# Kernel optimization log

Measured on AMD Instinct MI355X. Metric: run time of the kernel, lower is better.

## Reference

```python
import jax, jax.numpy as jnp
import numpy as np

B, N, D, H, NC = 4, 32, 128, 8, 27
DK = D // H
DFF = 4 * D
L = NC * N


def layer_norm(x, g, b, eps=1e-5):
    mu = jnp.mean(x, -1, keepdims=True)
    var = jnp.var(x, -1, keepdims=True)
    return (x - mu) * jax.lax.rsqrt(var + eps) * g + b


def setup_inputs() -> dict:
    ks = jax.random.split(jax.random.key(0), 16)
    s = 1.0 / np.sqrt(D)
    return {
        'x': jax.random.normal(ks[0], (B, N, D), jnp.float32),
        'mask': jax.random.randint(ks[1], (B, 1, N), 0, 2, jnp.int32),
        'coords': jax.random.normal(ks[2], (B, NC, N, 3), jnp.float32),
        'Wp': jax.random.normal(ks[3], (3, D), jnp.float32) * 0.5,
        'bp': jnp.zeros((D,), jnp.float32),
        'Wq': jax.random.normal(ks[4], (D, D), jnp.float32) * s,
        'bq': jnp.zeros((D,), jnp.float32),
        'Wk': jax.random.normal(ks[5], (D, D), jnp.float32) * s,
        'bk': jnp.zeros((D,), jnp.float32),
        'Wv': jax.random.normal(ks[6], (D, D), jnp.float32) * s,
        'bv': jnp.zeros((D,), jnp.float32),
        'Wo': jax.random.normal(ks[7], (D, D), jnp.float32) * s,
        'bo': jnp.zeros((D,), jnp.float32),
        'g1': jnp.ones((D,), jnp.float32),
        'b1': jnp.zeros((D,), jnp.float32),
        'g2': jnp.ones((D,), jnp.float32),
        'b2': jnp.zeros((D,), jnp.float32),
        'W1': jax.random.normal(ks[8], (D, DFF), jnp.float32) * s,
        'bf1': jnp.zeros((DFF,), jnp.float32),
        'W2': jax.random.normal(ks[9], (DFF, D), jnp.float32) * (1.0 / np.sqrt(DFF)),
        'bf2': jnp.zeros((D,), jnp.float32),
    }


def reference(x, mask, coords, Wp, bp, Wq, bq, Wk, bk, Wv, bv, Wo, bo,
              g1, b1, g2, b2, W1, bf1, W2, bf2):
    mask_enh = jnp.tile(mask, (1, NC, 1)).reshape(B, 1, 1, L)

    def step(i):
        # position_encoding: x broadcast over 27 images + linear of coords relative to atom i
        ci = jax.lax.dynamic_slice_in_dim(coords, i, 1, axis=2)        # [B,NC,1,3]
        ar = x[:, None] + (coords - ci) @ Wp + bp                      # [B,NC,N,D]
        a = ar.reshape(B, L, D)
        hn = layer_norm(a, g1, b1)
        q = (hn @ Wq + bq).reshape(B, L, H, DK).transpose(0, 2, 1, 3)
        k = (hn @ Wk + bk).reshape(B, L, H, DK).transpose(0, 2, 1, 3)
        v = (hn @ Wv + bv).reshape(B, L, H, DK).transpose(0, 2, 1, 3)
        scores = jnp.einsum('bhqd,bhkd->bhqk', q, k) / np.sqrt(DK)     # [B,H,L,L]
        scores = jnp.where(mask_enh == 0, -1e9, scores)
        att = jnp.einsum('bhqk,bhkd->bhqd', jax.nn.softmax(scores, -1), v)
        att = att.transpose(0, 2, 1, 3).reshape(B, L, D) @ Wo + bo
        s = a + att  # SublayerConnection (dropout identity in eval)
        # original keeps only [b, image 0, atom i] of the [B,NC,N,D] reshape; flat index = i
        return jax.lax.dynamic_slice_in_dim(s, i, 1, axis=1)[:, 0]     # [B,D]

    rows = jax.lax.map(step, jnp.arange(N))                            # [N,B,D]
    y = rows.transpose(1, 0, 2)                                        # [B,N,D]
    hn2 = layer_norm(y, g2, b2)
    return y + (jax.nn.relu(hn2 @ W1 + bf1) @ W2 + bf2)
```

## Files before the change

kernel.cpp:

```cpp
#include <hip/hip_runtime.h>


#define B_ 4
#define N_ 32
#define D_ 128
#define H_ 8
#define NC_ 27
#define DFF_ 512
#define L_ (NC_*N_)

__device__ __forceinline__ float wave_red_sum(float v){
  #pragma unroll
  for (int off = 32; off; off >>= 1) v += __shfl_xor(v, off);
  return v;
}

__device__ __forceinline__ void bred2(float& a, float& b, float sred[2][8][2],
                                      int tid, int phase){
  for (int off = 32; off; off >>= 1){ a += __shfl_xor(a, off); b += __shfl_xor(b, off); }
  int pb = phase & 1;
  if ((tid & 63) == 0){ sred[pb][tid>>6][0] = a; sred[pb][tid>>6][1] = b; }
  __syncthreads();
  float sa = 0.f, sb = 0.f;
  #pragma unroll
  for (int w = 0; w < 8; w++){ sa += sred[pb][w][0]; sb += sred[pb][w][1]; }
  a = sa; b = sb;
}

__global__ __launch_bounds__(512) void k_fused(
    const float* __restrict__ x, const int* __restrict__ mask,
    const float* __restrict__ coords,
    const float* __restrict__ Wp, const float* __restrict__ bp,
    const float* __restrict__ Wq, const float* __restrict__ bq,
    const float* __restrict__ Wk, const float* __restrict__ bk,
    const float* __restrict__ Wv, const float* __restrict__ bv,
    const float* __restrict__ Wo, const float* __restrict__ bo,
    const float* __restrict__ g1, const float* __restrict__ b1,
    const float* __restrict__ g2, const float* __restrict__ b2,
    const float* __restrict__ W1, const float* __restrict__ bf1,
    const float* __restrict__ W2, const float* __restrict__ bfb2,
    float* __restrict__ out)
{
  __shared__ float sc_s[H_*L_];
  __shared__ float is_s[L_];
  __shared__ float dc_s[3][L_];
  __shared__ float xh_s[N_][D_+1];
  __shared__ float ZU_s[H_][D_+4];
  __shared__ float w_s[3][D_];
  __shared__ float g1_s[D_], b1_s[D_], bp_s[D_];
  __shared__ float q_s[D_];
  __shared__ float hn_s[D_];
  __shared__ float qAxk_s[H_][N_];
  __shared__ float qGk_s[H_][3];
  __shared__ float S3_s[H_];
  __shared__ float varx_s[N_];
  __shared__ float dxp_s[N_][3];
  __shared__ int   mask_s[N_];
  __shared__ float cq_s[NC_][3];
  __shared__ float M6_s[6];
  __shared__ float mwp_s[3];
  __shared__ float Tnp_s[H_][2][N_];
  __shared__ float Sh_s[H_], RD_s[H_][3];
  __shared__ float att_s[D_], y_s[D_], f_s[DFF_];
  __shared__ float po[4][D_];
  __shared__ float sred[2][8][2];

  int bi = blockIdx.x;
  int b = bi >> 5, i = bi & 31;
  int tid  = threadIdx.x;
  int wave = tid >> 6, lane = tid & 63;

  if (tid < 384) w_s[tid>>7][tid&127] = Wp[tid];
  if (tid < D_){ g1_s[tid] = g1[tid]; b1_s[tid] = b1[tid]; bp_s[tid] = bp[tid]; }
  if (tid >= 384 && tid < 384+N_) mask_s[tid-384] = mask[b*N_ + (tid-384)];
  if (tid >= 416 && tid < 416+NC_*3){
    int t2 = tid - 416;
    cq_s[t2/3][t2%3] = coords[((size_t)(b*NC_ + t2/3)*N_ + i)*3 + t2%3];
  }
  __syncthreads();
  if (wave < 3){
    float s = w_s[wave][lane] + w_s[wave][lane+64];
    s = wave_red_sum(s);
    if (lane == 0) mwp_s[wave] = s*(1.f/D_);
  }
  __syncthreads();
  if (tid < 384) w_s[tid>>7][tid&127] -= mwp_s[tid>>7];
  __syncthreads();
  if (wave < 6){
    const int ja[6] = {0,0,0,1,1,2}, jb[6] = {0,1,2,1,2,2};
    float s = w_s[ja[wave]][lane]*w_s[jb[wave]][lane]
            + w_s[ja[wave]][lane+64]*w_s[jb[wave]][lane+64];
    s = wave_red_sum(s);
    if (lane == 0) M6_s[wave] = s;
  }

  for (int r = wave; r < N_; r += 8){
    float t0 = x[((size_t)(b*N_+r))*D_ + lane]     + bp_s[lane];
    float t1 = x[((size_t)(b*N_+r))*D_ + lane+64]  + bp_s[lane+64];
    float mean = wave_red_sum(t0 + t1)*(1.f/D_);
    float xh0 = t0 - mean, xh1 = t1 - mean;
    xh_s[r][lane] = xh0; xh_s[r][lane+64] = xh1;
    float vv = xh0*xh0 + xh1*xh1;
    float d0 = xh0*w_s[0][lane] + xh1*w_s[0][lane+64];
    float d1 = xh0*w_s[1][lane] + xh1*w_s[1][lane+64];
    float d2 = xh0*w_s[2][lane] + xh1*w_s[2][lane+64];
    #pragma unroll
    for (int off = 32; off; off >>= 1){
      vv += __shfl_xor(vv, off); d0 += __shfl_xor(d0, off);
      d1 += __shfl_xor(d1, off); d2 += __shfl_xor(d2, off);
    }
    if (lane == 0){
      varx_s[r] = vv*(1.f/D_);
      dxp_s[r][0] = d0; dxp_s[r][1] = d1; dxp_s[r][2] = d2;
    }
  }
  __syncthreads();

  if (tid < D_){
    float isq = rsqrtf(varx_s[i] + 1e-5f);
    hn_s[tid] = xh_s[i][tid]*isq*g1_s[tid] + b1_s[tid];
  }
  __syncthreads();
  {
    int slot = tid >> 7, d = tid & 127;
    float a = 0.f;
    #pragma unroll 8
    for (int e = slot*32; e < slot*32+32; e++) a += hn_s[e]*Wq[e*D_+d];
    po[slot][d] = a;
  }
  __syncthreads();
  if (tid < D_) q_s[tid] = po[0][tid]+po[1][tid]+po[2][tid]+po[3][tid] + bq[tid];
  __syncthreads();

  {
    int e = tid & 127, h0 = tid >> 7;
    #pragma unroll
    for (int hh = 0; hh < 2; hh++){
      int h = h0 + hh*4;
      const float4* wk4 = (const float4*)(Wk + (size_t)e*D_ + h*16);
      float s = 0.f;
      #pragma unroll
      for (int kq = 0; kq < 4; kq++){
        float4 wv4 = wk4[kq];
        s += wv4.x*q_s[h*16+kq*4+0] + wv4.y*q_s[h*16+kq*4+1]
           + wv4.z*q_s[h*16+kq*4+2] + wv4.w*q_s[h*16+kq*4+3];
      }
      ZU_s[h][e] = s;
    }
  }
  __syncthreads();
  {
    int h = wave;
    float u0 = ZU_s[h][lane], u1 = ZU_s[h][lane+64];
    float s3 = b1_s[lane]*u0 + b1_s[lane+64]*u1;
    if (lane < 16) s3 += q_s[h*16+lane]*bk[h*16+lane];
    float qg0 = w_s[0][lane]*g1_s[lane]*u0 + w_s[0][lane+64]*g1_s[lane+64]*u1;
    float qg1 = w_s[1][lane]*g1_s[lane]*u0 + w_s[1][lane+64]*g1_s[lane+64]*u1;
    float qg2 = w_s[2][lane]*g1_s[lane]*u0 + w_s[2][lane+64]*g1_s[lane+64]*u1;
    #pragma unroll
    for (int off = 32; off; off >>= 1){
      s3  += __shfl_xor(s3,  off); qg0 += __shfl_xor(qg0, off);
      qg1 += __shfl_xor(qg1, off); qg2 += __shfl_xor(qg2, off);
    }
    if (lane == 0){ S3_s[h]=s3; qGk_s[h][0]=qg0; qGk_s[h][1]=qg1; qGk_s[h][2]=qg2; }
  }
  __syncthreads();
  {
    int e = tid & 127, h0 = tid >> 7;
    ZU_s[h0][e]   *= g1_s[e];
    ZU_s[h0+4][e] *= g1_s[e];
  }
  __syncthreads();
  {
    int half = tid >> 8, id = tid & 255, h = id >> 5, n = id & 31;
    float s = 0.f;
    #pragma unroll 8
    for (int e = half*64; e < half*64+64; e++) s += xh_s[n][e]*ZU_s[h][e];
    ((float*)po)[half*256 + id] = s;
  }
  __syncthreads();
  if (tid < 256){
    int h = tid >> 5, n = tid & 31;
    qAxk_s[h][n] = ((float*)po)[tid] + ((float*)po)[256 + tid];
  }
  __syncthreads();

  for (int l = tid; l < L_; l += 512){
    int c = l >> 5, n = l & 31;
    const float* ck = coords + ((size_t)(b*NC_+c)*N_ + n)*3;
    float d0 = ck[0]-cq_s[c][0], d1 = ck[1]-cq_s[c][1], d2 = ck[2]-cq_s[c][2];
    dc_s[0][l] = d0; dc_s[1][l] = d1; dc_s[2][l] = d2;
    float quad = d0*d0*M6_s[0] + d1*d1*M6_s[3] + d2*d2*M6_s[5]
               + 2.f*(d0*d1*M6_s[1] + d0*d2*M6_s[2] + d1*d2*M6_s[4]);
    float lin  = d0*dxp_s[n][0] + d1*dxp_s[n][1] + d2*dxp_s[n][2];
    float E = varx_s[n] + (quad + 2.f*lin)*(1.f/D_);
    float is = rsqrtf(fmaxf(E, 0.f) + 1e-5f);
    is_s[l] = is;
    bool mk = mask_s[n] != 0;
    #pragma unroll
    for (int h = 0; h < H_; h++){
      float sc = 0.25f*(is*(qAxk_s[h][n]
                 + d0*qGk_s[h][0] + d1*qGk_s[h][1] + d2*qGk_s[h][2]) + S3_s[h]);
      sc_s[h*L_ + l] = mk ? sc : -1e9f;
    }
  }
  __syncthreads();

  {
    int h = tid >> 6, n = lane & 31, half = lane >> 5;
    int c0 = half ? 14 : 0, c1 = half ? NC_ : 14;
    float M = -3.0e38f;
    for (int c = c0; c < c1; c++) M = fmaxf(M, sc_s[h*L_ + c*N_ + n]);
    #pragma unroll
    for (int off = 32; off; off >>= 1) M = fmaxf(M, __shfl_xor(M, off));
    float S=0.f, Tn=0.f, r0=0.f, r1=0.f, r2=0.f;
    for (int c = c0; c < c1; c++){
      int l = c*N_ + n;
      float w = expf(sc_s[h*L_ + l] - M);
      float t = w * is_s[l];
      S += w; Tn += t;
      r0 += t*dc_s[0][l]; r1 += t*dc_s[1][l]; r2 += t*dc_s[2][l];
    }
    Tnp_s[h][half][n] = Tn;
    #pragma unroll
    for (int off = 32; off; off >>= 1){
      S  += __shfl_xor(S,  off);
      r0 += __shfl_xor(r0, off);
      r1 += __shfl_xor(r1, off);
      r2 += __shfl_xor(r2, off);
    }
    if (lane == 0){ Sh_s[h]=S; RD_s[h][0]=r0; RD_s[h][1]=r1; RD_s[h][2]=r2; }
  }
  __syncthreads();

  {
    int e = tid & 127, h0 = tid >> 7;
    #pragma unroll
    for (int hh = 0; hh < 2; hh++){
      int h = h0 + hh*4;
      float z = 0.f;
      #pragma unroll 8
      for (int n = 0; n < N_; n++){
        float Tn = Tnp_s[h][0][n] + Tnp_s[h][1][n];
        z += Tn * xh_s[n][e];
      }
      z += RD_s[h][0]*w_s[0][e] + RD_s[h][1]*w_s[1][e] + RD_s[h][2]*w_s[2][e];
      float rS = 1.f / fmaxf(Sh_s[h], 1e-30f);
      ZU_s[h][e] = z*g1_s[e]*rS + b1_s[e];
    }
  }
  __syncthreads();

  {
    int slot = tid >> 7, d = tid & 127, h = d >> 4;
    float a = 0.f;
    #pragma unroll 8
    for (int e = slot*32; e < slot*32+32; e++) a += ZU_s[h][e]*Wv[e*D_+d];
    po[slot][d] = a;
  }
  __syncthreads();
  if (tid < D_) att_s[tid] = po[0][tid]+po[1][tid]+po[2][tid]+po[3][tid] + bv[tid];
  __syncthreads();

  {
    int slot = tid >> 7, d = tid & 127;
    float a = 0.f;
    #pragma unroll 8
    for (int e = slot*32; e < slot*32+32; e++) a += att_s[e]*Wo[e*D_+d];
    po[slot][d] = a;
  }
  __syncthreads();
  float yv = 0.f;
  if (tid < D_){
    yv = x[(size_t)bi*D_+tid] + bp_s[tid] + bo[tid]
       + po[0][tid]+po[1][tid]+po[2][tid]+po[3][tid];
    y_s[tid] = yv;
  }
  float s1 = (tid < D_) ? yv : 0.f, dm = 0.f;
  bred2(s1, dm, sred, tid, 0);
  float dev = yv - s1*(1.f/D_);
  float v1 = (tid < D_) ? dev*dev : 0.f; dm = 0.f;
  bred2(v1, dm, sred, tid, 1);
  if (tid < D_) hn_s[tid] = dev*rsqrtf(v1*(1.f/D_)+1e-5f)*g2[tid] + b2[tid];
  __syncthreads();
  float f = bf1[tid];
  #pragma unroll 8
  for (int e = 0; e < D_; e++) f += hn_s[e]*W1[e*DFF_+tid];
  f_s[tid] = fmaxf(f, 0.f);
  __syncthreads();
  {
    int slot = tid >> 7, d = tid & 127;
    float a = 0.f;
    #pragma unroll 8
    for (int j = slot*128; j < slot*128+128; j++) a += f_s[j]*W2[j*D_+d];
    po[slot][d] = a;
  }
  __syncthreads();
  if (tid < D_)
    out[(size_t)bi*D_+tid] = y_s[tid] + bfb2[tid]
                   + po[0][tid]+po[1][tid]+po[2][tid]+po[3][tid];
}

extern "C" void kernel_launch(void* const* d_in, const int* in_sizes, int n_in,
                              void* d_out, int out_size, void* d_ws, size_t ws_size,
                              hipStream_t stream){
  const float* x      = (const float*)d_in[0];
  const int*   mask   = (const int*)  d_in[1];
  const float* coords = (const float*)d_in[2];
  const float* Wp     = (const float*)d_in[3];
  const float* bp     = (const float*)d_in[4];
  const float* Wq     = (const float*)d_in[5];
  const float* bq     = (const float*)d_in[6];
  const float* Wk     = (const float*)d_in[7];
  const float* bk     = (const float*)d_in[8];
  const float* Wv     = (const float*)d_in[9];
  const float* bv     = (const float*)d_in[10];
  const float* Wo     = (const float*)d_in[11];
  const float* bo     = (const float*)d_in[12];
  const float* g1     = (const float*)d_in[13];
  const float* b1     = (const float*)d_in[14];
  const float* g2     = (const float*)d_in[15];
  const float* b2     = (const float*)d_in[16];
  const float* W1     = (const float*)d_in[17];
  const float* bf1    = (const float*)d_in[18];
  const float* W2     = (const float*)d_in[19];
  const float* bfb2   = (const float*)d_in[20];

  k_fused<<<B_*N_, 512, 0, stream>>>(x, mask, coords, Wp, bp, Wq, bq, Wk, bk,
                                     Wv, bv, Wo, bo, g1, b1, g2, b2,
                                     W1, bf1, W2, bfb2, (float*)d_out);
}
```

Measured before the change: 125.6 us.

## Double block size to 1024 threads and merge dependent phases to cut barriers

Raises the fused kernel from 512 to 1024 threads per block and redistributes every phase (matvec K-splits into 8 slots, softmax split into 4 chunks per head with a separate max pass) across the extra waves. All global loads for x, coords and the small parameter vectors are issued up front into registers or shared memory. Several sequential barriered steps are merged: g1 is folded into xg/wcg, and the Wp mean is removed algebraically via P6. LayerNorm2 moves to a single wave. This is meant to shorten the serial latency chain of a 128-block kernel that underfills the GPU, at the cost of more registers per block and an extra barrier for the two-pass softmax max.

Measured after the change: 117.6 us. 1.07x faster.

```diff
diff --git a/kernel.cpp b/kernel.cpp
--- a/kernel.cpp
+++ b/kernel.cpp
@@ -9,25 +9,13 @@
 #define DFF_ 512
 #define L_ (NC_*N_)
 
-__device__ __forceinline__ float wave_red_sum(float v){
+__device__ __forceinline__ float wred(float v){
   #pragma unroll
   for (int off = 32; off; off >>= 1) v += __shfl_xor(v, off);
   return v;
 }
 
-__device__ __forceinline__ void bred2(float& a, float& b, float sred[2][8][2],
-                                      int tid, int phase){
-  for (int off = 32; off; off >>= 1){ a += __shfl_xor(a, off); b += __shfl_xor(b, off); }
-  int pb = phase & 1;
-  if ((tid & 63) == 0){ sred[pb][tid>>6][0] = a; sred[pb][tid>>6][1] = b; }
-  __syncthreads();
-  float sa = 0.f, sb = 0.f;
-  #pragma unroll
-  for (int w = 0; w < 8; w++){ sa += sred[pb][w][0]; sb += sred[pb][w][1]; }
-  a = sa; b = sb;
-}
-
-__global__ __launch_bounds__(512) void k_fused(
+__global__ __launch_bounds__(1024) void k_fused(
     const float* __restrict__ x, const int* __restrict__ mask,
     const float* __restrict__ coords,
     const float* __restrict__ Wp, const float* __restrict__ bp,
@@ -44,12 +32,13 @@
   __shared__ float sc_s[H_*L_];
   __shared__ float is_s[L_];
   __shared__ float dc_s[3][L_];
-  __shared__ float xh_s[N_][D_+1];
-  __shared__ float ZU_s[H_][D_+4];
+  __shared__ float xg_s[N_][D_+1];
+  __shared__ float zz_s[H_][D_+1];
   __shared__ float w_s[3][D_];
-  __shared__ float g1_s[D_], b1_s[D_], bp_s[D_];
-  __shared__ float q_s[D_];
-  __shared__ float hn_s[D_];
+  __shared__ float wcg_s[3][D_];
+  __shared__ float g1_s[D_], b1_s[D_], bp_s[D_], bq_s[D_], bk_s[D_];
+  __shared__ float g2_s[D_], b2_s[D_], bv_s[D_], bo_s[D_], bfb2_s[D_];
+  __shared__ float q_s[D_], hn_s[D_], hn2_s[D_], att_s[D_], y_s[D_];
   __shared__ float qAxk_s[H_][N_];
   __shared__ float qGk_s[H_][3];
   __shared__ float S3_s[H_];
@@ -57,248 +46,316 @@
   __shared__ float dxp_s[N_][3];
   __shared__ int   mask_s[N_];
   __shared__ float cq_s[NC_][3];
-  __shared__ float M6_s[6];
-  __shared__ float mwp_s[3];
+  __shared__ float M6_s[6], mwp_s[3], P6_s[6];
+  __shared__ float pmax_s[H_][2];
   __shared__ float Tnp_s[H_][2][N_];
-  __shared__ float Sh_s[H_], RD_s[H_][3];
-  __shared__ float att_s[D_], y_s[D_], f_s[DFF_];
-  __shared__ float po[4][D_];
-  __shared__ float sred[2][8][2];
+  __shared__ float Sp_s[H_][2], RDp_s[H_][2][3];
+  __shared__ float f_s[DFF_];
+  __shared__ float po[8][D_];
 
   int bi = blockIdx.x;
   int b = bi >> 5, i = bi & 31;
-  int tid  = threadIdx.x;
-  int wave = tid >> 6, lane = tid & 63;
-
+  int tid = threadIdx.x, wave = tid >> 6, lane = tid & 63;
+
+  int r0 = wave*2, r1 = wave*2+1;
+  float xa0 = x[(size_t)(b*N_+r0)*D_ + lane];
+  float xa1 = x[(size_t)(b*N_+r0)*D_ + lane+64];
+  float xb0 = x[(size_t)(b*N_+r1)*D_ + lane];
+  float xb1 = x[(size_t)(b*N_+r1)*D_ + lane+64];
+  float xi0 = 0.f, xi1 = 0.f;
+  if (wave == 0){ xi0 = x[(size_t)bi*D_+lane]; xi1 = x[(size_t)bi*D_+lane+64]; }
+  float ck0=0.f, ck1=0.f, ck2=0.f;
+  if (tid < L_){
+    int c = tid >> 5, n = tid & 31;
+    const float* ck = coords + ((size_t)(b*NC_+c)*N_ + n)*3;
+    ck0 = ck[0]; ck1 = ck[1]; ck2 = ck[2];
+  }
   if (tid < 384) w_s[tid>>7][tid&127] = Wp[tid];
-  if (tid < D_){ g1_s[tid] = g1[tid]; b1_s[tid] = b1[tid]; bp_s[tid] = bp[tid]; }
-  if (tid >= 384 && tid < 384+N_) mask_s[tid-384] = mask[b*N_ + (tid-384)];
-  if (tid >= 416 && tid < 416+NC_*3){
-    int t2 = tid - 416;
-    cq_s[t2/3][t2%3] = coords[((size_t)(b*NC_ + t2/3)*N_ + i)*3 + t2%3];
-  }
-  __syncthreads();
-  if (wave < 3){
-    float s = w_s[wave][lane] + w_s[wave][lane+64];
-    s = wave_red_sum(s);
-    if (lane == 0) mwp_s[wave] = s*(1.f/D_);
-  }
-  __syncthreads();
-  if (tid < 384) w_s[tid>>7][tid&127] -= mwp_s[tid>>7];
-  __syncthreads();
-  if (wave < 6){
-    const int ja[6] = {0,0,0,1,1,2}, jb[6] = {0,1,2,1,2,2};
-    float s = w_s[ja[wave]][lane]*w_s[jb[wave]][lane]
-            + w_s[ja[wave]][lane+64]*w_s[jb[wave]][lane+64];
-    s = wave_red_sum(s);
-    if (lane == 0) M6_s[wave] = s;
-  }
-
-  for (int r = wave; r < N_; r += 8){
-    float t0 = x[((size_t)(b*N_+r))*D_ + lane]     + bp_s[lane];
-    float t1 = x[((size_t)(b*N_+r))*D_ + lane+64]  + bp_s[lane+64];
-    float mean = wave_red_sum(t0 + t1)*(1.f/D_);
-    float xh0 = t0 - mean, xh1 = t1 - mean;
-    xh_s[r][lane] = xh0; xh_s[r][lane+64] = xh1;
-    float vv = xh0*xh0 + xh1*xh1;
-    float d0 = xh0*w_s[0][lane] + xh1*w_s[0][lane+64];
-    float d1 = xh0*w_s[1][lane] + xh1*w_s[1][lane+64];
-    float d2 = xh0*w_s[2][lane] + xh1*w_s[2][lane+64];
-    #pragma unroll
-    for (int off = 32; off; off >>= 1){
-      vv += __shfl_xor(vv, off); d0 += __shfl_xor(d0, off);
-      d1 += __shfl_xor(d1, off); d2 += __shfl_xor(d2, off);
-    }
-    if (lane == 0){
-      varx_s[r] = vv*(1.f/D_);
-      dxp_s[r][0] = d0; dxp_s[r][1] = d1; dxp_s[r][2] = d2;
-    }
+  if (tid < 128)                g2_s[tid]       = g2[tid];
+  else if (tid < 256)           b2_s[tid-128]   = b2[tid-128];
+  else if (tid < 384)           bv_s[tid-256]   = bv[tid-256];
+  else if (tid < 512){ int t=tid-384; g1_s[t]=g1[t]; bo_s[t]=bo[t]; }
+  else if (tid < 640){ int t=tid-512; b1_s[t]=b1[t]; bfb2_s[t]=bfb2[t]; }
+  else if (tid < 768){ int t=tid-640; bp_s[t]=bp[t]; bq_s[t]=bq[t]; }
+  else if (tid < 800)           mask_s[tid-768] = mask[b*N_ + (tid-768)];
+  else if (tid < 881){
+    int t = tid-800;
+    cq_s[t/3][t%3] = coords[((size_t)(b*NC_ + t/3)*N_ + i)*3 + t%3];
+  }
+  else if (tid < 1009)          bk_s[tid-881]   = bk[tid-881];
+  __syncthreads();
+
+  {
+    float t0 = xa0 + bp_s[lane], t1 = xa1 + bp_s[lane+64];
+    float mean = wred(t0+t1)*(1.f/D_);
+    float h0 = t0-mean, h1 = t1-mean;
+    xg_s[r0][lane]    = h0*g1_s[lane];
+    xg_s[r0][lane+64] = h1*g1_s[lane+64];
+    float vv = h0*h0 + h1*h1;
+    float d0 = h0*w_s[0][lane] + h1*w_s[0][lane+64];
+    float d1 = h0*w_s[1][lane] + h1*w_s[1][lane+64];
+    float d2 = h0*w_s[2][lane] + h1*w_s[2][lane+64];
+    #pragma unroll
+    for (int off=32; off; off>>=1){
+      vv += __shfl_xor(vv,off); d0 += __shfl_xor(d0,off);
+      d1 += __shfl_xor(d1,off); d2 += __shfl_xor(d2,off);
+    }
+    if (lane==0){ varx_s[r0]=vv*(1.f/D_);
+      dxp_s[r0][0]=d0; dxp_s[r0][1]=d1; dxp_s[r0][2]=d2; }
+    t0 = xb0 + bp_s[lane]; t1 = xb1 + bp_s[lane+64];
+    mean = wred(t0+t1)*(1.f/D_);
+    h0 = t0-mean; h1 = t1-mean;
+    xg_s[r1][lane]    = h0*g1_s[lane];
+    xg_s[r1][lane+64] = h1*g1_s[lane+64];
+    vv = h0*h0 + h1*h1;
+    d0 = h0*w_s[0][lane] + h1*w_s[0][lane+64];
+    d1 = h0*w_s[1][lane] + h1*w_s[1][lane+64];
+    d2 = h0*w_s[2][lane] + h1*w_s[2][lane+64];
+    #pragma unroll
+    for (int off=32; off; off>>=1){
+      vv += __shfl_xor(vv,off); d0 += __shfl_xor(d0,off);
+      d1 += __shfl_xor(d1,off); d2 += __shfl_xor(d2,off);
+    }
+    if (lane==0){ varx_s[r1]=vv*(1.f/D_);
+      dxp_s[r1][0]=d0; dxp_s[r1][1]=d1; dxp_s[r1][2]=d2; }
+  }
+  float dc0=0.f, dc1=0.f, dc2=0.f;
+  if (tid < L_){
+    int c = tid >> 5;
+    dc0 = ck0 - cq_s[c][0]; dc1 = ck1 - cq_s[c][1]; dc2 = ck2 - cq_s[c][2];
+    dc_s[0][tid]=dc0; dc_s[1][tid]=dc1; dc_s[2][tid]=dc2;
+  }
+  if (wave >= 8 && wave < 11){
+    int j = wave - 8;
+    float s = w_s[j][lane] + w_s[j][lane+64];
+    s = wred(s);
+    if (lane==0) mwp_s[j] = s*(1.f/D_);
+  }
+  if (wave >= 10){
+    int idx = wave - 10;
+    int ja = (idx>=3) + (idx>=5);
+    int jb = idx - (idx>=3)*2 - (idx>=5);
+    float s = w_s[ja][lane]*w_s[jb][lane] + w_s[ja][lane+64]*w_s[jb][lane+64];
+    s = wred(s);
+    if (lane==0) P6_s[idx] = s;
+  }
+  __syncthreads();
+
+  if (tid < 384){ int j=tid>>7, e=tid&127;
+    wcg_s[j][e] = (w_s[j][e] - mwp_s[j])*g1_s[e]; }
+  if (tid == 384){
+    M6_s[0]=P6_s[0]-D_*mwp_s[0]*mwp_s[0];
+    M6_s[1]=P6_s[1]-D_*mwp_s[0]*mwp_s[1];
+    M6_s[2]=P6_s[2]-D_*mwp_s[0]*mwp_s[2];
+    M6_s[3]=P6_s[3]-D_*mwp_s[1]*mwp_s[1];
+    M6_s[4]=P6_s[4]-D_*mwp_s[1]*mwp_s[2];
+    M6_s[5]=P6_s[5]-D_*mwp_s[2]*mwp_s[2];
+  }
+  if (tid >= 512 && tid < 640){ int e = tid-512;
+    hn_s[e] = xg_s[i][e]*rsqrtf(varx_s[i]+1e-5f) + b1_s[e]; }
+  __syncthreads();
+
+  {
+    int slot = tid>>7, d = tid&127;
+    float a = 0.f;
+    #pragma unroll
+    for (int e = slot*16; e < slot*16+16; e++) a += hn_s[e]*Wq[e*D_+d];
+    po[slot][d] = a;
   }
   __syncthreads();
 
   if (tid < D_){
-    float isq = rsqrtf(varx_s[i] + 1e-5f);
-    hn_s[tid] = xh_s[i][tid]*isq*g1_s[tid] + b1_s[tid];
-  }
-  __syncthreads();
-  {
-    int slot = tid >> 7, d = tid & 127;
-    float a = 0.f;
-    #pragma unroll 8
-    for (int e = slot*32; e < slot*32+32; e++) a += hn_s[e]*Wq[e*D_+d];
-    po[slot][d] = a;
-  }
-  __syncthreads();
-  if (tid < D_) q_s[tid] = po[0][tid]+po[1][tid]+po[2][tid]+po[3][tid] + bq[tid];
-  __syncthreads();
-
-  {
-    int e = tid & 127, h0 = tid >> 7;
-    #pragma unroll
-    for (int hh = 0; hh < 2; hh++){
-      int h = h0 + hh*4;
-      const float4* wk4 = (const float4*)(Wk + (size_t)e*D_ + h*16);
-      float s = 0.f;
-      #pragma unroll
-      for (int kq = 0; kq < 4; kq++){
-        float4 wv4 = wk4[kq];
-        s += wv4.x*q_s[h*16+kq*4+0] + wv4.y*q_s[h*16+kq*4+1]
-           + wv4.z*q_s[h*16+kq*4+2] + wv4.w*q_s[h*16+kq*4+3];
-      }
-      ZU_s[h][e] = s;
-    }
-  }
-  __syncthreads();
-  {
-    int h = wave;
-    float u0 = ZU_s[h][lane], u1 = ZU_s[h][lane+64];
-    float s3 = b1_s[lane]*u0 + b1_s[lane+64]*u1;
-    if (lane < 16) s3 += q_s[h*16+lane]*bk[h*16+lane];
-    float qg0 = w_s[0][lane]*g1_s[lane]*u0 + w_s[0][lane+64]*g1_s[lane+64]*u1;
-    float qg1 = w_s[1][lane]*g1_s[lane]*u0 + w_s[1][lane+64]*g1_s[lane+64]*u1;
-    float qg2 = w_s[2][lane]*g1_s[lane]*u0 + w_s[2][lane+64]*g1_s[lane+64]*u1;
-    #pragma unroll
-    for (int off = 32; off; off >>= 1){
-      s3  += __shfl_xor(s3,  off); qg0 += __shfl_xor(qg0, off);
-      qg1 += __shfl_xor(qg1, off); qg2 += __shfl_xor(qg2, off);
-    }
-    if (lane == 0){ S3_s[h]=s3; qGk_s[h][0]=qg0; qGk_s[h][1]=qg1; qGk_s[h][2]=qg2; }
-  }
-  __syncthreads();
-  {
-    int e = tid & 127, h0 = tid >> 7;
-    ZU_s[h0][e]   *= g1_s[e];
-    ZU_s[h0+4][e] *= g1_s[e];
-  }
-  __syncthreads();
-  {
-    int half = tid >> 8, id = tid & 255, h = id >> 5, n = id & 31;
+    float a = bq_s[tid];
+    #pragma unroll
+    for (int s=0;s<8;s++) a += po[s][tid];
+    q_s[tid] = a;
+  }
+  __syncthreads();
+
+  {
+    int h = tid>>7, e = tid&127;
+    const float4* wk4 = (const float4*)(Wk + (size_t)e*D_ + h*16);
+    float s = 0.f;
+    #pragma unroll
+    for (int kq=0; kq<4; kq++){
+      float4 w4 = wk4[kq];
+      s += w4.x*q_s[h*16+kq*4+0] + w4.y*q_s[h*16+kq*4+1]
+         + w4.z*q_s[h*16+kq*4+2] + w4.w*q_s[h*16+kq*4+3];
+    }
+    zz_s[h][e] = s;
+  }
+  __syncthreads();
+
+  {
+    int quarter = tid>>8, id = tid&255, h = id>>5, n = id&31;
     float s = 0.f;
     #pragma unroll 8
-    for (int e = half*64; e < half*64+64; e++) s += xh_s[n][e]*ZU_s[h][e];
-    ((float*)po)[half*256 + id] = s;
-  }
-  __syncthreads();
+    for (int e = quarter*32; e < quarter*32+32; e++) s += xg_s[n][e]*zz_s[h][e];
+    ((float*)po)[quarter*256 + id] = s;
+  }
+  __syncthreads();
+
   if (tid < 256){
-    int h = tid >> 5, n = tid & 31;
-    qAxk_s[h][n] = ((float*)po)[tid] + ((float*)po)[256 + tid];
-  }
-  __syncthreads();
-
-  for (int l = tid; l < L_; l += 512){
-    int c = l >> 5, n = l & 31;
-    const float* ck = coords + ((size_t)(b*NC_+c)*N_ + n)*3;
-    float d0 = ck[0]-cq_s[c][0], d1 = ck[1]-cq_s[c][1], d2 = ck[2]-cq_s[c][2];
-    dc_s[0][l] = d0; dc_s[1][l] = d1; dc_s[2][l] = d2;
-    float quad = d0*d0*M6_s[0] + d1*d1*M6_s[3] + d2*d2*M6_s[5]
-               + 2.f*(d0*d1*M6_s[1] + d0*d2*M6_s[2] + d1*d2*M6_s[4]);
-    float lin  = d0*dxp_s[n][0] + d1*dxp_s[n][1] + d2*dxp_s[n][2];
+    int h = tid>>5, n = tid&31;
+    qAxk_s[h][n] = ((float*)po)[tid] + ((float*)po)[256+tid]
+                 + ((float*)po)[512+tid] + ((float*)po)[768+tid];
+  }
+  if (wave >= 8){
+    int h = wave - 8;
+    float u0 = zz_s[h][lane], u1 = zz_s[h][lane+64];
+    float s3 = b1_s[lane]*u0 + b1_s[lane+64]*u1;
+    if (lane < 16) s3 += q_s[h*16+lane]*bk_s[h*16+lane];
+    float qg0 = wcg_s[0][lane]*u0 + wcg_s[0][lane+64]*u1;
+    float qg1 = wcg_s[1][lane]*u0 + wcg_s[1][lane+64]*u1;
+    float qg2 = wcg_s[2][lane]*u0 + wcg_s[2][lane+64]*u1;
+    #pragma unroll
+    for (int off=32; off; off>>=1){
+      s3  += __shfl_xor(s3,off);  qg0 += __shfl_xor(qg0,off);
+      qg1 += __shfl_xor(qg1,off); qg2 += __shfl_xor(qg2,off);
+    }
+    if (lane==0){ S3_s[h]=s3; qGk_s[h][0]=qg0; qGk_s[h][1]=qg1; qGk_s[h][2]=qg2; }
+  }
+  __syncthreads();
+
+  if (tid < L_){
+    int n = tid & 31;
+    float quad = dc0*dc0*M6_s[0] + dc1*dc1*M6_s[3] + dc2*dc2*M6_s[5]
+               + 2.f*(dc0*dc1*M6_s[1] + dc0*dc2*M6_s[2] + dc1*dc2*M6_s[4]);
+    float lin  = dc0*dxp_s[n][0] + dc1*dxp_s[n][1] + dc2*dxp_s[n][2];
     float E = varx_s[n] + (quad + 2.f*lin)*(1.f/D_);
     float is = rsqrtf(fmaxf(E, 0.f) + 1e-5f);
-    is_s[l] = is;
+    is_s[tid] = is;
     bool mk = mask_s[n] != 0;
     #pragma unroll
-    for (int h = 0; h < H_; h++){
+    for (int h=0; h<H_; h++){
       float sc = 0.25f*(is*(qAxk_s[h][n]
-                 + d0*qGk_s[h][0] + d1*qGk_s[h][1] + d2*qGk_s[h][2]) + S3_s[h]);
-      sc_s[h*L_ + l] = mk ? sc : -1e9f;
-    }
-  }
-  __syncthreads();
-
-  {
-    int h = tid >> 6, n = lane & 31, half = lane >> 5;
-    int c0 = half ? 14 : 0, c1 = half ? NC_ : 14;
+               + dc0*qGk_s[h][0] + dc1*qGk_s[h][1] + dc2*qGk_s[h][2]) + S3_s[h]);
+      sc_s[h*L_ + tid] = mk ? sc : -1e9f;
+    }
+  }
+  __syncthreads();
+
+  int h2 = wave>>1, sub = wave&1, n2 = lane&31, half2 = lane>>5;
+  int q4 = sub*2 + half2, c0 = q4*7, c1 = (q4==3) ? NC_ : c0+7;
+  {
     float M = -3.0e38f;
-    for (int c = c0; c < c1; c++) M = fmaxf(M, sc_s[h*L_ + c*N_ + n]);
-    #pragma unroll
-    for (int off = 32; off; off >>= 1) M = fmaxf(M, __shfl_xor(M, off));
-    float S=0.f, Tn=0.f, r0=0.f, r1=0.f, r2=0.f;
-    for (int c = c0; c < c1; c++){
-      int l = c*N_ + n;
-      float w = expf(sc_s[h*L_ + l] - M);
-      float t = w * is_s[l];
-      S += w; Tn += t;
-      r0 += t*dc_s[0][l]; r1 += t*dc_s[1][l]; r2 += t*dc_s[2][l];
-    }
-    Tnp_s[h][half][n] = Tn;
-    #pragma unroll
-    for (int off = 32; off; off >>= 1){
-      S  += __shfl_xor(S,  off);
-      r0 += __shfl_xor(r0, off);
-      r1 += __shfl_xor(r1, off);
-      r2 += __shfl_xor(r2, off);
-    }
-    if (lane == 0){ Sh_s[h]=S; RD_s[h][0]=r0; RD_s[h][1]=r1; RD_s[h][2]=r2; }
-  }
-  __syncthreads();
-
-  {
-    int e = tid & 127, h0 = tid >> 7;
-    #pragma unroll
-    for (int hh = 0; hh < 2; hh++){
-      int h = h0 + hh*4;
-      float z = 0.f;
-      #pragma unroll 8
-      for (int n = 0; n < N_; n++){
-        float Tn = Tnp_s[h][0][n] + Tnp_s[h][1][n];
-        z += Tn * xh_s[n][e];
-      }
-      z += RD_s[h][0]*w_s[0][e] + RD_s[h][1]*w_s[1][e] + RD_s[h][2]*w_s[2][e];
-      float rS = 1.f / fmaxf(Sh_s[h], 1e-30f);
-      ZU_s[h][e] = z*g1_s[e]*rS + b1_s[e];
-    }
-  }
-  __syncthreads();
-
-  {
-    int slot = tid >> 7, d = tid & 127, h = d >> 4;
+    for (int c=c0; c<c1; c++) M = fmaxf(M, sc_s[h2*L_ + c*N_ + n2]);
+    #pragma unroll
+    for (int off=32; off; off>>=1) M = fmaxf(M, __shfl_xor(M, off));
+    if (lane==0) pmax_s[h2][sub] = M;
+  }
+  __syncthreads();
+
+  {
+    float M = fmaxf(pmax_s[h2][0], pmax_s[h2][1]);
+    float S=0.f, Tn=0.f, rr0=0.f, rr1=0.f, rr2=0.f;
+    for (int c=c0; c<c1; c++){
+      int l = c*N_ + n2;
+      float w_ = __expf(sc_s[h2*L_ + l] - M);
+      float t = w_ * is_s[l];
+      S += w_; Tn += t;
+      rr0 += t*dc_s[0][l]; rr1 += t*dc_s[1][l]; rr2 += t*dc_s[2][l];
+    }
+    float Tn2 = Tn + __shfl_xor(Tn, 32);
+    if (lane < 32) Tnp_s[h2][sub][lane] = Tn2;
+    #pragma unroll
+    for (int off=32; off; off>>=1){
+      S   += __shfl_xor(S,off);   rr0 += __shfl_xor(rr0,off);
+      rr1 += __shfl_xor(rr1,off); rr2 += __shfl_xor(rr2,off);
+    }
+    if (lane==0){ Sp_s[h2][sub]=S;
+      RDp_s[h2][sub][0]=rr0; RDp_s[h2][sub][1]=rr1; RDp_s[h2][sub][2]=rr2; }
+  }
+  __syncthreads();
+
+  {
+    int h = tid>>7, e = tid&127;
+    float rS = 1.f / fmaxf(Sp_s[h][0]+Sp_s[h][1], 1e-30f);
+    float z = 0.f;
+    #pragma unroll 8
+    for (int n=0; n<N_; n++){
+      float Tn = Tnp_s[h][0][n] + Tnp_s[h][1][n];
+      z += Tn * xg_s[n][e];
+    }
+    float R0 = RDp_s[h][0][0]+RDp_s[h][1][0];
+    float R1 = RDp_s[h][0][1]+RDp_s[h][1][1];
+    float R2 = RDp_s[h][0][2]+RDp_s[h][1][2];
+    z += R0*wcg_s[0][e] + R1*wcg_s[1][e] + R2*wcg_s[2][e];
+    zz_s[h][e] = z*rS + b1_s[e];
+  }
+  __syncthreads();
+
+  {
+    int slot = tid>>7, d = tid&127, h = d>>4;
     float a = 0.f;
-    #pragma unroll 8
-    for (int e = slot*32; e < slot*32+32; e++) a += ZU_s[h][e]*Wv[e*D_+d];
+    #pragma unroll
+    for (int e = slot*16; e < slot*16+16; e++) a += zz_s[h][e]*Wv[e*D_+d];
     po[slot][d] = a;
   }
   __syncthreads();
-  if (tid < D_) att_s[tid] = po[0][tid]+po[1][tid]+po[2][tid]+po[3][tid] + bv[tid];
-  __syncthreads();
-
-  {
-    int slot = tid >> 7, d = tid & 127;
+
+  if (tid < D_){
+    float a = bv_s[tid];
+    #pragma unroll
+    for (int s=0;s<8;s++) a += po[s][tid];
+    att_s[tid] = a;
+  }
+  __syncthreads();
+
+  {
+    int slot = tid>>7, d = tid&127;
     float a = 0.f;
-    #pragma unroll 8
-    for (int e = slot*32; e < slot*32+32; e++) a += att_s[e]*Wo[e*D_+d];
+    #pragma unroll
+    for (int e = slot*16; e < slot*16+16; e++) a += att_s[e]*Wo[e*D_+d];
     po[slot][d] = a;
   }
   __syncthreads();
-  float yv = 0.f;
+
+  if (wave == 0){
+    float y0 = xi0 + bp_s[lane]    + bo_s[lane];
+    float y1 = xi1 + bp_s[lane+64] + bo_s[lane+64];
+    #pragma unroll
+    for (int s=0;s<8;s++){ y0 += po[s][lane]; y1 += po[s][lane+64]; }
+    y_s[lane] = y0; y_s[lane+64] = y1;
+    float mean = wred(y0+y1)*(1.f/D_);
+    float v0 = y0-mean, v1 = y1-mean;
+    float var = wred(v0*v0+v1*v1)*(1.f/D_);
+    float isd = rsqrtf(var + 1e-5f);
+    hn2_s[lane]    = v0*isd*g2_s[lane]    + b2_s[lane];
+    hn2_s[lane+64] = v1*isd*g2_s[lane+64] + b2_s[lane+64];
+  }
+  __syncthreads();
+
+  {
+    int col = tid&511, half = tid>>9;
+    float a = half ? 0.f : bf1[col];
+    #pragma unroll 16
+    for (int e = half*64; e < half*64+64; e++)
+      a += hn2_s[e]*W1[(size_t)e*DFF_ + col];
+    ((float*)po)[tid] = a;
+  }
+  __syncthreads();
+
+  if (tid < DFF_)
+    f_s[tid] = fmaxf(((float*)po)[tid] + ((float*)po)[DFF_+tid], 0.f);
+  __syncthreads();
+
+  {
+    int slot = tid>>7, d = tid&127;
+    float a = 0.f;
+    #pragma unroll 16
+    for (int j = slot*64; j < slot*64+64; j++)
+      a += f_s[j]*W2[(size_t)j*D_ + d];
+    po[slot][d] = a;
+  }
+  __syncthreads();
+
   if (tid < D_){
-    yv = x[(size_t)bi*D_+tid] + bp_s[tid] + bo[tid]
-       + po[0][tid]+po[1][tid]+po[2][tid]+po[3][tid];
-    y_s[tid] = yv;
-  }
-  float s1 = (tid < D_) ? yv : 0.f, dm = 0.f;
-  bred2(s1, dm, sred, tid, 0);
-  float dev = yv - s1*(1.f/D_);
-  float v1 = (tid < D_) ? dev*dev : 0.f; dm = 0.f;
-  bred2(v1, dm, sred, tid, 1);
-  if (tid < D_) hn_s[tid] = dev*rsqrtf(v1*(1.f/D_)+1e-5f)*g2[tid] + b2[tid];
-  __syncthreads();
-  float f = bf1[tid];
-  #pragma unroll 8
-  for (int e = 0; e < D_; e++) f += hn_s[e]*W1[e*DFF_+tid];
-  f_s[tid] = fmaxf(f, 0.f);
-  __syncthreads();
-  {
-    int slot = tid >> 7, d = tid & 127;
-    float a = 0.f;
-    #pragma unroll 8
-    for (int j = slot*128; j < slot*128+128; j++) a += f_s[j]*W2[j*D_+d];
-    po[slot][d] = a;
-  }
-  __syncthreads();
-  if (tid < D_)
-    out[(size_t)bi*D_+tid] = y_s[tid] + bfb2[tid]
-                   + po[0][tid]+po[1][tid]+po[2][tid]+po[3][tid];
+    float a = y_s[tid] + bfb2_s[tid];
+    #pragma unroll
+    for (int s=0;s<8;s++) a += po[s][tid];
+    out[(size_t)bi*D_ + tid] = a;
+  }
 }
 
 extern "C" void kernel_launch(void* const* d_in, const int* in_sizes, int n_in,
@@ -326,7 +383,7 @@
   const float* W2     = (const float*)d_in[19];
   const float* bfb2   = (const float*)d_in[20];
 
-  k_fused<<<B_*N_, 512, 0, stream>>>(x, mask, coords, Wp, bp, Wq, bq, Wk, bk,
-                                     Wv, bv, Wo, bo, g1, b1, g2, b2,
-                                     W1, bf1, W2, bfb2, (float*)d_out);
+  k_fused<<<B_*N_, 1024, 0, stream>>>(x, mask, coords, Wp, bp, Wq, bq, Wk, bk,
+                                      Wv, bv, Wo, bo, g1, b1, g2, b2,
+                                      W1, bf1, W2, bfb2, (float*)d_out);
 }
```
